# Optimization experiments

Measured on AMD Instinct MI355X. Metric: run time of the kernel, lower is better.

## Reference

```python
import jax, jax.numpy as jnp
import numpy as np
from jax import lax

B, T, C_IN, C_OUT, H = 2048, 128, 2, 16, 232


def setup_inputs() -> dict:
    key = jax.random.key(0)
    k0, k1, k2, k3 = jax.random.split(key, 4)
    X = jax.random.normal(k0, (B, T, C_IN), dtype=jnp.float32)
    # kaiming_normal init (fan_in mode) as in reset_parameters
    conv_w = jax.random.normal(k1, (C_OUT, C_IN, 3), dtype=jnp.float32) * np.sqrt(2.0 / (C_IN * 3))
    conv_b = jnp.zeros((C_OUT,), dtype=jnp.float32)
    w_ih = jax.random.normal(k2, (3 * H, C_OUT), dtype=jnp.float32) * np.sqrt(2.0 / C_OUT)
    w_hh = jax.random.normal(k3, (3 * H, H), dtype=jnp.float32) * np.sqrt(2.0 / H)
    b_ih = jnp.zeros((3 * H,), dtype=jnp.float32)
    b_hh = jnp.zeros((3 * H,), dtype=jnp.float32)
    return {"X": X, "conv_w": conv_w, "conv_b": conv_b,
            "w_ih": w_ih, "w_hh": w_hh, "b_ih": b_ih, "b_hh": b_hh}


def reference(X, conv_w, conv_b, w_ih, w_hh, b_ih, b_hh):
    # Conv1d(2->16, k=3, pad=1) on [B, C, T] + ReLU
    Xc = jnp.transpose(X, (0, 2, 1))                      # [B, 2, T]
    y = lax.conv_general_dilated(Xc, conv_w, window_strides=(1,),
                                 padding=[(1, 1)],
                                 dimension_numbers=("NCH", "OIH", "NCH"))
    y = jax.nn.relu(y + conv_b[None, :, None])            # [B, 16, T]
    x_embed = jnp.transpose(y, (0, 2, 1))                 # [B, T, 16]

    # GRU (torch gate order: r, z, n). Precompute input projections for all t.
    gi = jnp.einsum("btc,gc->btg", x_embed, w_ih) + b_ih  # [B, T, 3H]

    def step(h, g_t):
        gh = h @ w_hh.T + b_hh                            # [B, 3H]
        ir, iz, in_ = jnp.split(g_t, 3, axis=-1)
        hr, hz, hn = jnp.split(gh, 3, axis=-1)
        r = jax.nn.sigmoid(ir + hr)
        z = jax.nn.sigmoid(iz + hz)
        n = jnp.tanh(in_ + r * hn)
        h_new = (1.0 - z) * n + z * h
        return h_new, None

    h0 = jnp.zeros((X.shape[0], w_hh.shape[1]), dtype=X.dtype)
    hT, _ = lax.scan(step, h0, jnp.moveaxis(gi, 1, 0))    # final state [B, H]
    return hT
```

## Files before the change

kernel.cpp:

```cpp
#include <hip/hip_runtime.h>

#define BATCH 2048
#define T     128
#define CIN   2
#define COUT  16
#define H     232
#define RPB   8
#define NBLK  (BATCH/RPB)
#define NTHR  512
#define NGRP  15
#define NT2   48
#define NS    9
#define HROW  272

#define OFF_HA   0
#define SZ_HA    (2 * RPB * HROW * 2)
#define OFF_XE   (OFF_HA + SZ_HA)
#define SZ_XE    (T * RPB * 16 * 2)
#define OFF_WL   (OFF_XE + SZ_XE)
#define SZ_WL    (8 * 10 * 64 * 8 * 2)
#define OFF_CW   (OFF_WL + SZ_WL)
#define SZ_CW    512
#define SMEM_BYTES (OFF_CW + SZ_CW)

typedef _Float16 half8 __attribute__((ext_vector_type(8)));
typedef float  floatx4 __attribute__((ext_vector_type(4)));

#define MFMA __builtin_amdgcn_mfma_f32_16x16x32_f16

__device__ __align__(16) _Float16 g_packedW[NT2 * NS * 64 * 8];

__global__ void pack_w_kernel(const float* __restrict__ w_ih,
                              const float* __restrict__ w_hh) {
  int tile = blockIdx.x, slice = blockIdx.y, lane = threadIdx.x;
  int grp = tile / NGRP;
  int j   = (tile % NGRP) * 16 + (lane & 15);
  int g   = grp * H + j;
  bool valid = (tile < 3 * NGRP) && (j < H);
  half8 v = {};
  if (valid) {
#pragma unroll
    for (int i = 0; i < 8; ++i) {
      int k = slice * 32 + ((lane >> 4) << 3) + i;
      float f = 0.f;
      if (slice < 8) {
        if (k < H) f = w_hh[g * H + k];
        else if (k < H + COUT && grp < 2) f = w_ih[g * COUT + (k - H)];
      } else {
        int xk = k - 256;
        if (xk >= 0 && xk < COUT && grp == 2) f = w_ih[g * COUT + xk];
      }
      v[i] = (_Float16)f;
    }
  }
  *(half8*)&g_packedW[((tile * NS + slice) * 64 + lane) * 8] = v;
}

__device__ __forceinline__ float sigmoid_f(float x) {
  return __builtin_amdgcn_rcpf(1.f + __expf(-x));
}

__global__ __launch_bounds__(NTHR, 2) void st_gru_kernel(
    const float* __restrict__ X,
    const float* __restrict__ conv_w, const float* __restrict__ conv_b,
    const float* __restrict__ b_ih, const float* __restrict__ b_hh,
    float* __restrict__ out) {

  extern __shared__ __align__(16) char smem[];
  _Float16* hAflat = (_Float16*)(smem + OFF_HA);
  _Float16* Xemb   = (_Float16*)(smem + OFF_XE);
  _Float16* wLDS   = (_Float16*)(smem + OFF_WL);
  float*    cwp    = (float*)(smem + OFF_CW);

  const int tid  = threadIdx.x;
  const int lane = tid & 63;
  const int wave = tid >> 6;
  const int r_a  = lane & 15;
  const int ch4  = lane >> 4;
  const int blk  = blockIdx.x;
  const int rr   = r_a & 7;
  const int swz  = rr & 3;

  for (int i = tid; i < 2 * RPB * HROW; i += NTHR) hAflat[i] = (_Float16)0;
  if (tid < COUT * CIN * 3) cwp[tid] = conv_w[tid];
  if (tid < COUT) cwp[96 + tid] = conv_b[tid];
  __syncthreads();

  for (int p = tid; p < RPB * T; p += NTHR) {
    int r = p >> 7, t = p & (T - 1);
    const float* xr = X + (size_t)(blk * RPB + r) * (T * CIN);
    float x0[3], x1[3];
#pragma unroll
    for (int d = 0; d < 3; ++d) {
      int tt = t + d - 1;
      bool ok = (unsigned)tt < (unsigned)T;
      x0[d] = ok ? xr[tt * 2] : 0.f;
      x1[d] = ok ? xr[tt * 2 + 1] : 0.f;
    }
    half8 lo, hi;
#pragma unroll
    for (int c = 0; c < COUT; ++c) {
      float a = cwp[96 + c];
#pragma unroll
      for (int d = 0; d < 3; ++d)
        a += x0[d] * cwp[c * 6 + d] + x1[d] * cwp[c * 6 + 3 + d];
      _Float16 hv = (_Float16)fmaxf(a, 0.f);
      if (c < 8) lo[c] = hv; else hi[c - 8] = hv;
    }
    *(half8*)&Xemb[(t * RPB + r) * 16] = lo;
    *(half8*)&Xemb[(t * RPB + r) * 16 + 8] = hi;
  }

  const int gi0 = wave * 2, gi1 = wave * 2 + 1;
  const bool g1ok = (gi1 < NGRP);
  const int tr0 = gi0, tz0 = gi0 + NGRP, tn0 = gi0 + 2 * NGRP;
  const int tr1 = g1ok ? gi1 : 45, tz1 = g1ok ? gi1 + NGRP : 46, tn1 = g1ok ? gi1 + 2 * NGRP : 47;
  const half8* Wp = (const half8*)g_packedW;

  half8* myz = (half8*)(wLDS + wave * (10 * 64 * 8));
#pragma unroll
  for (int f = 0; f < 4; ++f) myz[f * 64 + lane] = Wp[(tz0 * NS + f) * 64 + lane];
#pragma unroll
  for (int f = 0; f < 4; ++f) myz[(4 + f) * 64 + lane] = Wp[(tz1 * NS + f) * 64 + lane];
  myz[8 * 64 + lane] = Wp[(tn0 * NS + 8) * 64 + lane];
  myz[9 * 64 + lane] = Wp[(tn1 * NS + 8) * 64 + lane];

  half8 wr0[8], wr1[8], wn0[8], wn1[8], wzh0[4], wzh1[4];
#pragma unroll
  for (int s = 0; s < 8; ++s) {
    wr0[s] = Wp[(tr0 * NS + s) * 64 + lane];
    wr1[s] = Wp[(tr1 * NS + s) * 64 + lane];
    wn0[s] = Wp[(tn0 * NS + s) * 64 + lane];
    wn1[s] = Wp[(tn1 * NS + s) * 64 + lane];
  }
#pragma unroll
  for (int s = 0; s < 4; ++s) {
    wzh0[s] = Wp[(tz0 * NS + 4 + s) * 64 + lane];
    wzh1[s] = Wp[(tz1 * NS + 4 + s) * 64 + lane];
  }

  const int j0 = gi0 * 16 + r_a, j1 = gi1 * 16 + r_a;
  float bsr0 = 0.f, bsz0 = 0.f, bin0 = 0.f, bhn0 = 0.f;
  float bsr1 = 0.f, bsz1 = 0.f, bin1 = 0.f, bhn1 = 0.f;
  if (j0 < H) {
    bsr0 = b_ih[j0] + b_hh[j0];
    bsz0 = b_ih[H + j0] + b_hh[H + j0];
    bin0 = b_ih[2 * H + j0]; bhn0 = b_hh[2 * H + j0];
  }
  if (g1ok && j1 < H) {
    bsr1 = b_ih[j1] + b_hh[j1];
    bsz1 = b_ih[H + j1] + b_hh[H + j1];
    bin1 = b_ih[2 * H + j1]; bhn1 = b_hh[2 * H + j1];
  }

  const int eb   = (ch4 & 2);
  const int rowb = ((ch4 & 1) << 2) | (ch4 & 2);

  int woff0[2], woff1[2];
#pragma unroll
  for (int u = 0; u < 2; ++u) {
    int row = rowb + u;
    woff0[u] = row * HROW + ((j0 & ~31) | ((((j0 >> 3) & 3) ^ (row & 3)) << 3) | (j0 & 7));
    woff1[u] = row * HROW + ((j1 & ~31) | ((((j1 >> 3) & 3) ^ (row & 3)) << 3) | (j1 & 7));
  }

  float h0[2] = {0.f, 0.f};
  float h1[2] = {0.f, 0.f};

  __syncthreads();

  const int abase = rr * HROW + ((ch4 ^ swz) << 3);

  for (int t = 0; t < T; ++t) {
    const _Float16* rb = hAflat + (t & 1) * (RPB * HROW);
    _Float16* wb = hAflat + ((t & 1) ^ 1) * (RPB * HROW);

    const _Float16* pa7 = (ch4 == 0)
        ? rb + rr * HROW + 224 + (swz << 3)
        : Xemb + (t * RPB + rr) * 16 + ((((ch4 - 1) & 1)) << 3);
    half8 A7 = *(const half8*)pa7;
    half8 A8 = *(const half8*)(Xemb + (t * RPB + rr) * 16 + ((ch4 & 1) << 3));

    floatx4 ra0 = {}, za0 = {}, na0 = {}, xa0 = {};
#pragma unroll
    for (int s = 0; s < 4; ++s) {
      half8 a = *(const half8*)&rb[abase + s * 32];
      ra0 = MFMA(a, wr0[s], ra0, 0, 0, 0);
      za0 = MFMA(a, myz[s * 64 + lane], za0, 0, 0, 0);
      na0 = MFMA(a, wn0[s], na0, 0, 0, 0);
    }
#pragma unroll
    for (int s = 4; s < 7; ++s) {
      half8 a = *(const half8*)&rb[abase + s * 32];
      ra0 = MFMA(a, wr0[s], ra0, 0, 0, 0);
      za0 = MFMA(a, wzh0[s - 4], za0, 0, 0, 0);
      na0 = MFMA(a, wn0[s], na0, 0, 0, 0);
    }
    ra0 = MFMA(A7, wr0[7], ra0, 0, 0, 0);
    za0 = MFMA(A7, wzh0[3], za0, 0, 0, 0);
    na0 = MFMA(A7, wn0[7], na0, 0, 0, 0);
    xa0 = MFMA(A8, myz[8 * 64 + lane], xa0, 0, 0, 0);

    floatx4 ra1 = {}, za1 = {}, na1 = {}, xa1 = {};
#pragma unroll
    for (int s = 0; s < 4; ++s) {
      half8 a = *(const half8*)&rb[abase + s * 32];
      ra1 = MFMA(a, wr1[s], ra1, 0, 0, 0);
      za1 = MFMA(a, myz[(4 + s) * 64 + lane], za1, 0, 0, 0);
      na1 = MFMA(a, wn1[s], na1, 0, 0, 0);
    }
#pragma unroll
    for (int s = 4; s < 7; ++s) {
      half8 a = *(const half8*)&rb[abase + s * 32];
      ra1 = MFMA(a, wr1[s], ra1, 0, 0, 0);
      za1 = MFMA(a, wzh1[s - 4], za1, 0, 0, 0);
      na1 = MFMA(a, wn1[s], na1, 0, 0, 0);
    }
    ra1 = MFMA(A7, wr1[7], ra1, 0, 0, 0);
    za1 = MFMA(A7, wzh1[3], za1, 0, 0, 0);
    na1 = MFMA(A7, wn1[7], na1, 0, 0, 0);
    xa1 = MFMA(A8, myz[9 * 64 + lane], xa1, 0, 0, 0);

#pragma unroll
    for (int u = 0; u < 2; ++u) {
      int e = eb + u;
      float r = sigmoid_f(ra0[e] + bsr0);
      float z = sigmoid_f(za0[e] + bsz0);
      float pre = xa0[e] + bin0 + r * (na0[e] + bhn0);
      float ee = __expf(2.f * pre);
      float n = 1.f - 2.f * __builtin_amdgcn_rcpf(ee + 1.f);
      h0[u] = n + z * (h0[u] - n);
      wb[woff0[u]] = (_Float16)h0[u];
    }
#pragma unroll
    for (int u = 0; u < 2; ++u) {
      int e = eb + u;
      float r = sigmoid_f(ra1[e] + bsr1);
      float z = sigmoid_f(za1[e] + bsz1);
      float pre = xa1[e] + bin1 + r * (na1[e] + bhn1);
      float ee = __expf(2.f * pre);
      float n = 1.f - 2.f * __builtin_amdgcn_rcpf(ee + 1.f);
      h1[u] = n + z * (h1[u] - n);
      wb[woff1[u]] = (_Float16)h1[u];
    }
    __syncthreads();
  }

#pragma unroll
  for (int u = 0; u < 2; ++u) {
    int row = rowb + u;
    if (j0 < H) out[(size_t)(blk * RPB + row) * H + j0] = h0[u];
    if (g1ok && j1 < H) out[(size_t)(blk * RPB + row) * H + j1] = h1[u];
  }
}

extern "C" void kernel_launch(void* const* d_in, const int* in_sizes, int n_in,
                              void* d_out, int out_size, void* d_ws, size_t ws_size,
                              hipStream_t stream) {
  const float* X      = (const float*)d_in[0];
  const float* conv_w = (const float*)d_in[1];
  const float* conv_b = (const float*)d_in[2];
  const float* w_ih   = (const float*)d_in[3];
  const float* w_hh   = (const float*)d_in[4];
  const float* b_ih   = (const float*)d_in[5];
  const float* b_hh   = (const float*)d_in[6];
  float* out = (float*)d_out;

  static bool attr_set = false;
  if (!attr_set) {
    hipFuncSetAttribute((const void*)st_gru_kernel,
                        hipFuncAttributeMaxDynamicSharedMemorySize, SMEM_BYTES);
    attr_set = true;
  }

  pack_w_kernel<<<dim3(NT2, NS), 64, 0, stream>>>(w_ih, w_hh);
  st_gru_kernel<<<NBLK, NTHR, SMEM_BYTES, stream>>>(X, conv_w, conv_b, b_ih, b_hh, out);
}
```

Baseline: 183.3 us.

## Unroll GRU time loop by two, interleave gate math with MFMAs, skip idle group

Unrolls the recurrent loop by two so the double-buffer offsets become compile-time constants, with incrementing pointers for the Xemb and A7 operands. All A-fragments are loaded up front and reused across both column groups. The sigmoid/tanh work for group 0 is interleaved between group 1's MFMAs to hide latency, and wave 7 skips its padding group entirely. More z-gate weight slices move from registers to LDS, which frees VGPRs but adds LDS reads per step.

```diff
diff --git a/kernel.cpp b/kernel.cpp
--- a/kernel.cpp
+++ b/kernel.cpp
@@ -12,16 +12,18 @@
 #define NT2   48
 #define NS    9
 #define HROW  272
+#define HBUF_H (RPB * HROW)
 
 #define OFF_HA   0
 #define SZ_HA    (2 * RPB * HROW * 2)
 #define OFF_XE   (OFF_HA + SZ_HA)
 #define SZ_XE    (T * RPB * 16 * 2)
 #define OFF_WL   (OFF_XE + SZ_XE)
-#define SZ_WL    (8 * 10 * 64 * 8 * 2)
+#define SZ_WL    (8 * 14 * 64 * 8 * 2)
 #define OFF_CW   (OFF_WL + SZ_WL)
 #define SZ_CW    512
 #define SMEM_BYTES (OFF_CW + SZ_CW)
+#define OFF_XE_H (OFF_XE / 2)
 
 typedef _Float16 half8 __attribute__((ext_vector_type(8)));
 typedef float  floatx4 __attribute__((ext_vector_type(4)));
@@ -67,6 +69,7 @@
     float* __restrict__ out) {
 
   extern __shared__ __align__(16) char smem[];
+  _Float16* lds16  = (_Float16*)smem;
   _Float16* hAflat = (_Float16*)(smem + OFF_HA);
   _Float16* Xemb   = (_Float16*)(smem + OFF_XE);
   _Float16* wLDS   = (_Float16*)(smem + OFF_WL);
@@ -117,15 +120,15 @@
   const int tr1 = g1ok ? gi1 : 45, tz1 = g1ok ? gi1 + NGRP : 46, tn1 = g1ok ? gi1 + 2 * NGRP : 47;
   const half8* Wp = (const half8*)g_packedW;
 
-  half8* myz = (half8*)(wLDS + wave * (10 * 64 * 8));
-#pragma unroll
-  for (int f = 0; f < 4; ++f) myz[f * 64 + lane] = Wp[(tz0 * NS + f) * 64 + lane];
-#pragma unroll
-  for (int f = 0; f < 4; ++f) myz[(4 + f) * 64 + lane] = Wp[(tz1 * NS + f) * 64 + lane];
-  myz[8 * 64 + lane] = Wp[(tn0 * NS + 8) * 64 + lane];
-  myz[9 * 64 + lane] = Wp[(tn1 * NS + 8) * 64 + lane];
-
-  half8 wr0[8], wr1[8], wn0[8], wn1[8], wzh0[4], wzh1[4];
+  half8* myz = (half8*)(wLDS + wave * (14 * 64 * 8));
+#pragma unroll
+  for (int f = 0; f < 6; ++f) myz[f * 64 + lane] = Wp[(tz0 * NS + f) * 64 + lane];
+#pragma unroll
+  for (int f = 0; f < 6; ++f) myz[(6 + f) * 64 + lane] = Wp[(tz1 * NS + f) * 64 + lane];
+  myz[12 * 64 + lane] = Wp[(tn0 * NS + 8) * 64 + lane];
+  myz[13 * 64 + lane] = Wp[(tn1 * NS + 8) * 64 + lane];
+
+  half8 wr0[8], wr1[8], wn0[8], wn1[8], wzh0[2], wzh1[2];
 #pragma unroll
   for (int s = 0; s < 8; ++s) {
     wr0[s] = Wp[(tr0 * NS + s) * 64 + lane];
@@ -133,11 +136,10 @@
     wn0[s] = Wp[(tn0 * NS + s) * 64 + lane];
     wn1[s] = Wp[(tn1 * NS + s) * 64 + lane];
   }
-#pragma unroll
-  for (int s = 0; s < 4; ++s) {
-    wzh0[s] = Wp[(tz0 * NS + 4 + s) * 64 + lane];
-    wzh1[s] = Wp[(tz1 * NS + 4 + s) * 64 + lane];
-  }
+  wzh0[0] = Wp[(tz0 * NS + 6) * 64 + lane];
+  wzh0[1] = Wp[(tz0 * NS + 7) * 64 + lane];
+  wzh1[0] = Wp[(tz1 * NS + 6) * 64 + lane];
+  wzh1[1] = Wp[(tz1 * NS + 7) * 64 + lane];
 
   const int j0 = gi0 * 16 + r_a, j1 = gi1 * 16 + r_a;
   float bsr0 = 0.f, bsz0 = 0.f, bin0 = 0.f, bhn0 = 0.f;
@@ -167,84 +169,103 @@
   float h0[2] = {0.f, 0.f};
   float h1[2] = {0.f, 0.f};
 
+  const int aoff = rr * HROW + ((ch4 ^ swz) << 3);
+  const int inc7 = (ch4 == 0) ? 0 : 256;
+  int pa7_e = (ch4 == 0) ? (0      + rr * HROW + 224 + (swz << 3))
+                         : (OFF_XE_H + rr * 16 + ((ch4 == 2) ? 8 : 0));
+  int pa7_o = (ch4 == 0) ? (HBUF_H + rr * HROW + 224 + (swz << 3))
+                         : (OFF_XE_H + 128 + rr * 16 + ((ch4 == 2) ? 8 : 0));
+  int a8i = OFF_XE_H + rr * 16 + ((ch4 & 1) << 3);
+
   __syncthreads();
 
-  const int abase = rr * HROW + ((ch4 ^ swz) << 3);
-
-  for (int t = 0; t < T; ++t) {
-    const _Float16* rb = hAflat + (t & 1) * (RPB * HROW);
-    _Float16* wb = hAflat + ((t & 1) ^ 1) * (RPB * HROW);
-
-    const _Float16* pa7 = (ch4 == 0)
-        ? rb + rr * HROW + 224 + (swz << 3)
-        : Xemb + (t * RPB + rr) * 16 + ((((ch4 - 1) & 1)) << 3);
-    half8 A7 = *(const half8*)pa7;
-    half8 A8 = *(const half8*)(Xemb + (t * RPB + rr) * 16 + ((ch4 & 1) << 3));
-
-    floatx4 ra0 = {}, za0 = {}, na0 = {}, xa0 = {};
-#pragma unroll
-    for (int s = 0; s < 4; ++s) {
-      half8 a = *(const half8*)&rb[abase + s * 32];
-      ra0 = MFMA(a, wr0[s], ra0, 0, 0, 0);
-      za0 = MFMA(a, myz[s * 64 + lane], za0, 0, 0, 0);
-      na0 = MFMA(a, wn0[s], na0, 0, 0, 0);
-    }
-#pragma unroll
-    for (int s = 4; s < 7; ++s) {
-      half8 a = *(const half8*)&rb[abase + s * 32];
-      ra0 = MFMA(a, wr0[s], ra0, 0, 0, 0);
-      za0 = MFMA(a, wzh0[s - 4], za0, 0, 0, 0);
-      na0 = MFMA(a, wn0[s], na0, 0, 0, 0);
-    }
-    ra0 = MFMA(A7, wr0[7], ra0, 0, 0, 0);
-    za0 = MFMA(A7, wzh0[3], za0, 0, 0, 0);
-    na0 = MFMA(A7, wn0[7], na0, 0, 0, 0);
-    xa0 = MFMA(A8, myz[8 * 64 + lane], xa0, 0, 0, 0);
-
-    floatx4 ra1 = {}, za1 = {}, na1 = {}, xa1 = {};
-#pragma unroll
-    for (int s = 0; s < 4; ++s) {
-      half8 a = *(const half8*)&rb[abase + s * 32];
-      ra1 = MFMA(a, wr1[s], ra1, 0, 0, 0);
-      za1 = MFMA(a, myz[(4 + s) * 64 + lane], za1, 0, 0, 0);
-      na1 = MFMA(a, wn1[s], na1, 0, 0, 0);
-    }
-#pragma unroll
-    for (int s = 4; s < 7; ++s) {
-      half8 a = *(const half8*)&rb[abase + s * 32];
-      ra1 = MFMA(a, wr1[s], ra1, 0, 0, 0);
-      za1 = MFMA(a, wzh1[s - 4], za1, 0, 0, 0);
-      na1 = MFMA(a, wn1[s], na1, 0, 0, 0);
-    }
-    ra1 = MFMA(A7, wr1[7], ra1, 0, 0, 0);
-    za1 = MFMA(A7, wzh1[3], za1, 0, 0, 0);
-    na1 = MFMA(A7, wn1[7], na1, 0, 0, 0);
-    xa1 = MFMA(A8, myz[9 * 64 + lane], xa1, 0, 0, 0);
-
-#pragma unroll
-    for (int u = 0; u < 2; ++u) {
-      int e = eb + u;
-      float r = sigmoid_f(ra0[e] + bsr0);
-      float z = sigmoid_f(za0[e] + bsz0);
-      float pre = xa0[e] + bin0 + r * (na0[e] + bhn0);
-      float ee = __expf(2.f * pre);
-      float n = 1.f - 2.f * __builtin_amdgcn_rcpf(ee + 1.f);
-      h0[u] = n + z * (h0[u] - n);
-      wb[woff0[u]] = (_Float16)h0[u];
-    }
-#pragma unroll
-    for (int u = 0; u < 2; ++u) {
-      int e = eb + u;
-      float r = sigmoid_f(ra1[e] + bsr1);
-      float z = sigmoid_f(za1[e] + bsz1);
-      float pre = xa1[e] + bin1 + r * (na1[e] + bhn1);
-      float ee = __expf(2.f * pre);
-      float n = 1.f - 2.f * __builtin_amdgcn_rcpf(ee + 1.f);
-      h1[u] = n + z * (h1[u] - n);
-      wb[woff1[u]] = (_Float16)h1[u];
-    }
-    __syncthreads();
-  }
+#define GRU_STEP(RBH, WBH, PA7, A8I) do {                                      \
+    half8 A_[7];                                                               \
+    _Pragma("unroll")                                                          \
+    for (int s = 0; s < 7; ++s)                                                \
+      A_[s] = *(const half8*)&lds16[(RBH) + aoff + s * 32];                    \
+    half8 A7_ = *(const half8*)&lds16[(PA7)];                                  \
+    half8 A8_ = *(const half8*)&lds16[(A8I)];                                  \
+    floatx4 ra0 = {}, za0 = {}, na0 = {}, xa0 = {};                            \
+    _Pragma("unroll")                                                          \
+    for (int s = 0; s < 6; ++s) {                                              \
+      ra0 = MFMA(A_[s], wr0[s], ra0, 0, 0, 0);                                 \
+      za0 = MFMA(A_[s], myz[s * 64 + lane], za0, 0, 0, 0);                     \
+      na0 = MFMA(A_[s], wn0[s], na0, 0, 0, 0);                                 \
+    }                                                                          \
+    ra0 = MFMA(A_[6], wr0[6], ra0, 0, 0, 0);                                   \
+    za0 = MFMA(A_[6], wzh0[0], za0, 0, 0, 0);                                  \
+    na0 = MFMA(A_[6], wn0[6], na0, 0, 0, 0);                                   \
+    ra0 = MFMA(A7_, wr0[7], ra0, 0, 0, 0);                                     \
+    za0 = MFMA(A7_, wzh0[1], za0, 0, 0, 0);                                    \
+    na0 = MFMA(A7_, wn0[7], na0, 0, 0, 0);                                     \
+    xa0 = MFMA(A8_, myz[12 * 64 + lane], xa0, 0, 0, 0);                        \
+    if (g1ok) {                                                                \
+      floatx4 ra1 = {}, za1 = {}, na1 = {}, xa1 = {};                          \
+      _Pragma("unroll")                                                        \
+      for (int s = 0; s < 4; ++s) {                                            \
+        ra1 = MFMA(A_[s], wr1[s], ra1, 0, 0, 0);                               \
+        za1 = MFMA(A_[s], myz[(6 + s) * 64 + lane], za1, 0, 0, 0);             \
+        na1 = MFMA(A_[s], wn1[s], na1, 0, 0, 0);                               \
+      }                                                                        \
+      float sr_[2], sz_[2];                                                    \
+      _Pragma("unroll")                                                        \
+      for (int u = 0; u < 2; ++u) {                                            \
+        sr_[u] = sigmoid_f(ra0[eb + u] + bsr0);                                \
+        sz_[u] = sigmoid_f(za0[eb + u] + bsz0);                                \
+      }                                                                        \
+      _Pragma("unroll")                                                        \
+      for (int s = 4; s < 6; ++s) {                                            \
+        ra1 = MFMA(A_[s], wr1[s], ra1, 0, 0, 0);                               \
+        za1 = MFMA(A_[s], myz[(6 + s) * 64 + lane], za1, 0, 0, 0);             \
+        na1 = MFMA(A_[s], wn1[s], na1, 0, 0, 0);                               \
+      }                                                                        \
+      ra1 = MFMA(A_[6], wr1[6], ra1, 0, 0, 0);                                 \
+      za1 = MFMA(A_[6], wzh1[0], za1, 0, 0, 0);                                \
+      na1 = MFMA(A_[6], wn1[6], na1, 0, 0, 0);                                 \
+      _Pragma("unroll")                                                        \
+      for (int u = 0; u < 2; ++u) {                                            \
+        float pre = xa0[eb + u] + bin0 + sr_[u] * (na0[eb + u] + bhn0);        \
+        float ee = __expf(2.f * pre);                                          \
+        float n = 1.f - 2.f * __builtin_amdgcn_rcpf(ee + 1.f);                 \
+        h0[u] = n + sz_[u] * (h0[u] - n);                                      \
+        lds16[(WBH) + woff0[u]] = (_Float16)h0[u];                             \
+      }                                                                        \
+      ra1 = MFMA(A7_, wr1[7], ra1, 0, 0, 0);                                   \
+      za1 = MFMA(A7_, wzh1[1], za1, 0, 0, 0);                                  \
+      na1 = MFMA(A7_, wn1[7], na1, 0, 0, 0);                                   \
+      xa1 = MFMA(A8_, myz[13 * 64 + lane], xa1, 0, 0, 0);                      \
+      _Pragma("unroll")                                                        \
+      for (int u = 0; u < 2; ++u) {                                            \
+        float r = sigmoid_f(ra1[eb + u] + bsr1);                               \
+        float z = sigmoid_f(za1[eb + u] + bsz1);                               \
+        float pre = xa1[eb + u] + bin1 + r * (na1[eb + u] + bhn1);             \
+        float ee = __expf(2.f * pre);                                          \
+        float n = 1.f - 2.f * __builtin_amdgcn_rcpf(ee + 1.f);                 \
+        h1[u] = n + z * (h1[u] - n);                                           \
+        lds16[(WBH) + woff1[u]] = (_Float16)h1[u];                             \
+      }                                                                        \
+    } else {                                                                   \
+      _Pragma("unroll")                                                        \
+      for (int u = 0; u < 2; ++u) {                                            \
+        float r = sigmoid_f(ra0[eb + u] + bsr0);                               \
+        float z = sigmoid_f(za0[eb + u] + bsz0);                               \
+        float pre = xa0[eb + u] + bin0 + r * (na0[eb + u] + bhn0);             \
+        float ee = __expf(2.f * pre);                                          \
+        float n = 1.f - 2.f * __builtin_amdgcn_rcpf(ee + 1.f);                 \
+        h0[u] = n + z * (h0[u] - n);                                           \
+        lds16[(WBH) + woff0[u]] = (_Float16)h0[u];                             \
+      }                                                                        \
+    }                                                                          \
+    __syncthreads();                                                           \
+  } while (0)
+
+  for (int tt = 0; tt < T; tt += 2) {
+    GRU_STEP(0,      HBUF_H, pa7_e, a8i);
+    GRU_STEP(HBUF_H, 0,      pa7_o, a8i + 128);
+    pa7_e += inc7; pa7_o += inc7; a8i += 256;
+  }
+#undef GRU_STEP
 
 #pragma unroll
   for (int u = 0; u < 2; ++u) {
```

Result: no change. 185.7 us (+1.3%).
